# Optimization experiments

Measured on AMD Instinct MI355X. Metric: run time of the kernel, lower is better.

Reference implementation:

```python
import jax, jax.numpy as jnp
import numpy as np

EMBED = 1024
HEADS = 16
HDIM = EMBED // HEADS
WIN = 14
RANK = 16
ALPHA = 32
MLP = 4 * EMBED


def setup_inputs() -> dict:
    key = jax.random.key(0)
    ks = jax.random.split(key, 10)
    s = 0.02
    return {
        "x": jax.random.normal(ks[0], (2, 64, 64, EMBED), jnp.float32),
        "norm1_g": jnp.ones((EMBED,), jnp.float32),
        "norm1_b": jnp.zeros((EMBED,), jnp.float32),
        "qkv_w": jax.random.normal(ks[1], (EMBED, 3 * EMBED), jnp.float32) * s,
        "qkv_b": jnp.zeros((3 * EMBED,), jnp.float32),
        "lora_a": jax.random.normal(ks[2], (EMBED, RANK), jnp.float32) * s,
        "lora_b": jax.random.normal(ks[3], (RANK, 3 * EMBED), jnp.float32) * s,
        "rel_pos_h": jax.random.normal(ks[4], (2 * WIN - 1, HDIM), jnp.float32) * s,
        "rel_pos_w": jax.random.normal(ks[5], (2 * WIN - 1, HDIM), jnp.float32) * s,
        "proj_w": jax.random.normal(ks[6], (EMBED, EMBED), jnp.float32) * s,
        "proj_b": jnp.zeros((EMBED,), jnp.float32),
        "norm2_g": jnp.ones((EMBED,), jnp.float32),
        "norm2_b": jnp.zeros((EMBED,), jnp.float32),
        "mlp_w1": jax.random.normal(ks[7], (EMBED, MLP), jnp.float32) * s,
        "mlp_b1": jnp.zeros((MLP,), jnp.float32),
        "mlp_w2": jax.random.normal(ks[8], (MLP, EMBED), jnp.float32) * s,
        "mlp_b2": jnp.zeros((EMBED,), jnp.float32),
    }


def layer_norm(x, g, b, eps=1e-6):
    mu = jnp.mean(x, axis=-1, keepdims=True)
    var = jnp.var(x, axis=-1, keepdims=True)
    return (x - mu) * jax.lax.rsqrt(var + eps) * g + b


def window_partition(x, w):
    B, H, W, C = x.shape
    ph, pw = (w - H % w) % w, (w - W % w) % w
    x = jnp.pad(x, ((0, 0), (0, ph), (0, pw), (0, 0)))
    Hp, Wp = H + ph, W + pw
    x = x.reshape(B, Hp // w, w, Wp // w, w, C)
    x = x.transpose(0, 1, 3, 2, 4, 5).reshape(-1, w, w, C)
    return x, (Hp, Wp)


def window_unpartition(x, w, pad_hw, hw):
    Hp, Wp = pad_hw
    H, W = hw
    B = x.shape[0] // (Hp // w * (Wp // w))
    x = x.reshape(B, Hp // w, Wp // w, w, w, -1)
    x = x.transpose(0, 1, 3, 2, 4, 5).reshape(B, Hp, Wp, -1)
    return x[:, :H, :W, :]


def _rel_table(rel_pos, size):
    # square windows, no interpolation: table is (2*size-1, dim)
    idx = jnp.arange(size)[:, None] - jnp.arange(size)[None, :] + (size - 1)
    return rel_pos[idx]  # (size, size, dim)


def reference(x, norm1_g, norm1_b, qkv_w, qkv_b, lora_a, lora_b,
              rel_pos_h, rel_pos_w, proj_w, proj_b, norm2_g, norm2_b,
              mlp_w1, mlp_b1, mlp_w2, mlp_b2):
    shortcut = x
    xn = layer_norm(x, norm1_g, norm1_b)
    h, w = xn.shape[1], xn.shape[2]
    xw, pad_hw = window_partition(xn, WIN)
    Bw, H, W, C = xw.shape
    N = H * W
    xf = xw.reshape(Bw, N, C)
    # QKV with LoRA injection: qkv(x) + (x @ A @ B) * alpha/rank
    qkv = xf @ qkv_w + qkv_b + (xf @ lora_a @ lora_b) * (ALPHA / RANK)
    qkv = qkv.reshape(Bw, N, 3, HEADS, HDIM).transpose(2, 0, 3, 1, 4)  # 3,Bw,h,N,d
    q, k, v = qkv[0], qkv[1], qkv[2]
    scale = HDIM ** -0.5
    attn = jnp.einsum('bhnd,bhmd->bhnm', q * scale, k)  # (Bw,heads,N,N)
    # decomposed relative position bias
    Rh = _rel_table(rel_pos_h, H)  # (H,H,d)
    Rw = _rel_table(rel_pos_w, W)  # (W,W,d)
    rq = q.reshape(Bw, HEADS, H, W, HDIM)
    rel_h = jnp.einsum('bhxyd,xkd->bhxyk', rq, Rh)  # (Bw,heads,H,W,H)
    rel_w = jnp.einsum('bhxyd,ykd->bhxyk', rq, Rw)  # (Bw,heads,H,W,W)
    attn = (attn.reshape(Bw, HEADS, H, W, H, W)
            + rel_h[..., :, None] + rel_w[..., None, :]).reshape(Bw, HEADS, N, N)
    attn = jax.nn.softmax(attn, axis=-1)
    out = jnp.einsum('bhnm,bhmd->bhnd', attn, v)
    out = out.reshape(Bw, HEADS, H, W, HDIM).transpose(0, 2, 3, 1, 4).reshape(Bw, H, W, C)
    out = out @ proj_w + proj_b
    out = window_unpartition(out, WIN, pad_hw, (h, w))
    x = shortcut + out
    # MLP with exact GELU (torch default)
    xn2 = layer_norm(x, norm2_g, norm2_b)
    hmid = jax.nn.gelu(xn2 @ mlp_w1 + mlp_b1, approximate=False)
    x = x + (hmid @ mlp_w2 + mlp_b2)
    return x
```

## Files before the change

### kernel.cpp

```cpp
#include <hip/hip_runtime.h>
#include <cstdint>
#include <cstddef>


typedef __bf16 bf16x8 __attribute__((ext_vector_type(8)));
typedef float f32x4 __attribute__((ext_vector_type(4)));

__device__ __forceinline__ unsigned short f2bf(float f) {
    unsigned u = __float_as_uint(f);
    u = (u + 0x7fffu + ((u >> 16) & 1u)) >> 16;
    return (unsigned short)u;
}
__device__ __forceinline__ float bf2f(unsigned short h) {
    return __uint_as_float(((unsigned)h) << 16);
}

#define GLDS16(gp, lp) __builtin_amdgcn_global_load_lds( \
    (__attribute__((address_space(1))) unsigned int*)(gp), \
    (__attribute__((address_space(3))) unsigned int*)(lp), 16, 0, 0)

__global__ __launch_bounds__(256) void weff_kernel(
    const float* __restrict__ W, const float* __restrict__ la,
    const float* __restrict__ lb, unsigned short* __restrict__ Wt)
{
    __shared__ float tile[32][33];
    __shared__ float lat[32][16];
    __shared__ float lbt[16][32];
    const int kb = blockIdx.x * 32, nb = blockIdx.y * 32;
    const int tn = threadIdx.x & 31, tk = threadIdx.x >> 5;
    for (int i = threadIdx.x; i < 32 * 16; i += 256)
        lat[i >> 4][i & 15] = la[(size_t)(kb + (i >> 4)) * 16 + (i & 15)];
    for (int i = threadIdx.x; i < 16 * 32; i += 256)
        lbt[i >> 5][i & 31] = lb[(size_t)(i >> 5) * 3072 + nb + (i & 31)];
#pragma unroll
    for (int i = 0; i < 4; ++i) {
        int k = tk + i * 8;
        tile[k][tn] = W[(size_t)(kb + k) * 3072 + nb + tn];
    }
    __syncthreads();
#pragma unroll
    for (int i = 0; i < 4; ++i) {
        int n = tk + i * 8;
        float acc = tile[tn][n];
#pragma unroll
        for (int r = 0; r < 16; ++r) acc += 2.0f * lat[tn][r] * lbt[r][n];
        Wt[(size_t)(nb + n) * 1024 + kb + tn] = f2bf(acc);
    }
}

__global__ __launch_bounds__(256) void transpose_bf16_kernel(
    const float* __restrict__ W, unsigned short* __restrict__ Wt,
    int Kdim, int Ndim)
{
    __shared__ float tile[32][33];
    const int kb = blockIdx.x * 32, nb = blockIdx.y * 32;
    const int tn = threadIdx.x & 31, tk = threadIdx.x >> 5;
#pragma unroll
    for (int i = 0; i < 4; ++i) {
        int k = tk + i * 8;
        tile[k][tn] = W[(size_t)(kb + k) * Ndim + nb + tn];
    }
    __syncthreads();
#pragma unroll
    for (int i = 0; i < 4; ++i) {
        int n = tk + i * 8;
        Wt[(size_t)(nb + n) * Kdim + kb + tn] = f2bf(tile[tn][n]);
    }
}

__global__ __launch_bounds__(256) void ln1_kernel(
    const float* __restrict__ x, const float* __restrict__ g,
    const float* __restrict__ b, unsigned short* __restrict__ out)
{
    const int blk = blockIdx.x;
    const int tid = threadIdx.x;
    const int bw = blk / 196, tok = blk - bw * 196;
    const int bat = bw / 25, rw = bw - bat * 25;
    const int wy = rw / 5, wx = rw - wy * 5;
    const int ty = tok / 14, tx = tok - ty * 14;
    const int y = wy * 14 + ty, xx = wx * 14 + tx;
    unsigned short* orow = out + (size_t)blk * 1024;
    if (y >= 64 || xx >= 64) {
        *(uint2*)(orow + tid * 4) = make_uint2(0u, 0u);
        return;
    }
    const float* irow = x + ((size_t)((bat * 64 + y) * 64 + xx)) * 1024;
    const float4 v = *(const float4*)(irow + tid * 4);
    float s = v.x + v.y + v.z + v.w;
    float ss = v.x * v.x + v.y * v.y + v.z * v.z + v.w * v.w;
    for (int o = 32; o > 0; o >>= 1) { s += __shfl_xor(s, o); ss += __shfl_xor(ss, o); }
    __shared__ float red[8];
    const int wave = tid >> 6, lane = tid & 63;
    if (lane == 0) { red[wave] = s; red[4 + wave] = ss; }
    __syncthreads();
    s = red[0] + red[1] + red[2] + red[3];
    ss = red[4] + red[5] + red[6] + red[7];
    const float mu = s * (1.0f / 1024.0f);
    const float var = ss * (1.0f / 1024.0f) - mu * mu;
    const float rstd = rsqrtf(var + 1e-6f);
    const float4 gv = *(const float4*)(g + tid * 4);
    const float4 bv = *(const float4*)(b + tid * 4);
    const float a0 = (v.x - mu) * rstd * gv.x + bv.x;
    const float a1 = (v.y - mu) * rstd * gv.y + bv.y;
    const float a2 = (v.z - mu) * rstd * gv.z + bv.z;
    const float a3 = (v.w - mu) * rstd * gv.w + bv.w;
    const unsigned r0 = (unsigned)f2bf(a0) | ((unsigned)f2bf(a1) << 16);
    const unsigned r1 = (unsigned)f2bf(a2) | ((unsigned)f2bf(a3) << 16);
    *(uint2*)(orow + tid * 4) = make_uint2(r0, r1);
}

__global__ __launch_bounds__(256) void ln2_kernel(
    const float* __restrict__ x, const float* __restrict__ g,
    const float* __restrict__ b, unsigned short* __restrict__ out)
{
    const int blk = blockIdx.x;
    const int tid = threadIdx.x;
    const float* irow = x + (size_t)blk * 1024;
    unsigned short* orow = out + (size_t)blk * 1024;
    const float4 v = *(const float4*)(irow + tid * 4);
    float s = v.x + v.y + v.z + v.w;
    float ss = v.x * v.x + v.y * v.y + v.z * v.z + v.w * v.w;
    for (int o = 32; o > 0; o >>= 1) { s += __shfl_xor(s, o); ss += __shfl_xor(ss, o); }
    __shared__ float red[8];
    const int wave = tid >> 6, lane = tid & 63;
    if (lane == 0) { red[wave] = s; red[4 + wave] = ss; }
    __syncthreads();
    s = red[0] + red[1] + red[2] + red[3];
    ss = red[4] + red[5] + red[6] + red[7];
    const float mu = s * (1.0f / 1024.0f);
    const float var = ss * (1.0f / 1024.0f) - mu * mu;
    const float rstd = rsqrtf(var + 1e-6f);
    const float4 gv = *(const float4*)(g + tid * 4);
    const float4 bv = *(const float4*)(b + tid * 4);
    const float a0 = (v.x - mu) * rstd * gv.x + bv.x;
    const float a1 = (v.y - mu) * rstd * gv.y + bv.y;
    const float a2 = (v.z - mu) * rstd * gv.z + bv.z;
    const float a3 = (v.w - mu) * rstd * gv.w + bv.w;
    const unsigned r0 = (unsigned)f2bf(a0) | ((unsigned)f2bf(a1) << 16);
    const unsigned r1 = (unsigned)f2bf(a2) | ((unsigned)f2bf(a3) << 16);
    *(uint2*)(orow + tid * 4) = make_uint2(r0, r1);
}

template <int EPI, int KS>
__global__ __launch_bounds__(512, 2) void gemm8p_v3(
    const unsigned short* __restrict__ A,
    const unsigned short* __restrict__ Bt,
    const float* __restrict__ bias,
    void* __restrict__ outp,
    int M, int K, int nbm, int nbn)
{
    __shared__ unsigned short As_s[2 * 16384];
    __shared__ unsigned short Bs_s[2 * 16384];

    const int tid = threadIdx.x;
    const int wave = tid >> 6, lane = tid & 63;
    const int lr = lane & 15, lq = lane >> 4;

    const int ss = (nbm + 7) >> 3;
    const int xcd = blockIdx.x & 7;
    const int sidx = blockIdx.x >> 3;
    const int ntl2 = sidx / ss;
    const int m_loc = sidx - ntl2 * ss;
    const int mt = xcd * ss + m_loc;
    if (mt >= nbm) return;
    int ks = 0, ntl = ntl2;
    if constexpr (KS > 1) { ks = ntl2 / nbn; ntl = ntl2 - ks * nbn; }
    const int m_base = mt * 256, n_base = ntl * 256;
    const int Kp = K / KS, kb = ks * Kp;
    const int NT = Kp >> 6;

    const int wm = (wave >> 2) * 128;
    const int wn = (wave & 3) * 64;

    const int srow = tid >> 3, sslot = tid & 7;
    const int gch = sslot ^ (srow & 7);
    const unsigned short* a_gp[4];
    const unsigned short* b_gp[4];
#pragma unroll
    for (int u = 0; u < 4; ++u) {
        int ar = m_base + u * 64 + srow; ar = ar < M ? ar : M - 1;
        a_gp[u] = A + (size_t)ar * K + kb + gch * 8;
        b_gp[u] = Bt + (size_t)(n_base + u * 64 + srow) * K + kb + gch * 8;
    }
#define STG_A(t, u) GLDS16(a_gp[u] + (size_t)(t) * 64, As_s + (((t) & 1) << 14) + (u) * 4096 + tid * 8)
#define STG_B(t, u) GLDS16(b_gp[u] + (size_t)(t) * 64, Bs_s + (((t) & 1) << 14) + (u) * 4096 + tid * 8)

    const int sl0 = lq ^ (lr & 7);
    const int a_off = (wm + lr) * 64 + sl0 * 8;
    const int b_off = (wn + lr) * 64 + sl0 * 8;

    f32x4 acc[8][4] = {};

    STG_A(0, 0); STG_A(0, 2);
    STG_B(0, 0); STG_B(0, 1); STG_B(0, 2); STG_B(0, 3);
    STG_A(0, 1); STG_A(0, 3);
    asm volatile("s_waitcnt vmcnt(2)" ::: "memory");
    __builtin_amdgcn_s_barrier();

    for (int t = 0; t < NT; ++t) {
        const unsigned short* Ab = As_s + ((t & 1) << 14);
        const unsigned short* Bb = Bs_s + ((t & 1) << 14);
        bf16x8 af[4], bfv[4];
#pragma unroll
        for (int mf = 0; mf < 4; ++mf) af[mf] = *(const bf16x8*)(Ab + a_off + mf * 1024);
#pragma unroll
        for (int nf = 0; nf < 4; ++nf) bfv[nf] = *(const bf16x8*)(Bb + b_off + nf * 1024);
        if (t + 1 < NT) { STG_A(t + 1, 0); STG_A(t + 1, 2); }
        __builtin_amdgcn_s_barrier();
        asm volatile("s_waitcnt lgkmcnt(0)" ::: "memory");
        __builtin_amdgcn_sched_barrier(0);
        __builtin_amdgcn_s_setprio(1);
#pragma unroll
        for (int mf = 0; mf < 4; ++mf)
#pragma unroll
            for (int nf = 0; nf < 4; ++nf)
                acc[mf][nf] = __builtin_amdgcn_mfma_f32_16x16x32_bf16(af[mf], bfv[nf], acc[mf][nf], 0, 0, 0);
        __builtin_amdgcn_s_setprio(0);
        __builtin_amdgcn_s_barrier();
#pragma unroll
        for (int mf = 0; mf < 4; ++mf) af[mf] = *(const bf16x8*)(Ab + (a_off ^ 32) + mf * 1024);
#pragma unroll
        for (int nf = 0; nf < 4; ++nf) bfv[nf] = *(const bf16x8*)(Bb + (b_off ^ 32) + nf * 1024);
        if (t + 1 < NT) { STG_B(t + 1, 0); STG_B(t + 1, 1); }
        __builtin_amdgcn_s_barrier();
        asm volatile("s_waitcnt lgkmcnt(0)" ::: "memory");
        __builtin_amdgcn_sched_barrier(0);
        __builtin_amdgcn_s_setprio(1);
#pragma unroll
        for (int mf = 0; mf < 4; ++mf)
#pragma unroll
            for (int nf = 0; nf < 4; ++nf)
                acc[mf][nf] = __builtin_amdgcn_mfma_f32_16x16x32_bf16(af[mf], bfv[nf], acc[mf][nf], 0, 0, 0);
        __builtin_amdgcn_s_setprio(0);
        if (t == NT - 1) { asm volatile("s_waitcnt vmcnt(0)" ::: "memory"); }
        else             { asm volatile("s_waitcnt vmcnt(4)" ::: "memory"); }
        __builtin_amdgcn_s_barrier();
#pragma unroll
        for (int mf = 0; mf < 4; ++mf) af[mf] = *(const bf16x8*)(Ab + a_off + (4 + mf) * 1024);
#pragma unroll
        for (int nf = 0; nf < 4; ++nf) bfv[nf] = *(const bf16x8*)(Bb + b_off + nf * 1024);
        if (t + 1 < NT) { STG_B(t + 1, 2); STG_B(t + 1, 3); }
        __builtin_amdgcn_s_barrier();
        asm volatile("s_waitcnt lgkmcnt(0)" ::: "memory");
        __builtin_amdgcn_sched_barrier(0);
        __builtin_amdgcn_s_setprio(1);
#pragma unroll
        for (int mf = 0; mf < 4; ++mf)
#pragma unroll
            for (int nf = 0; nf < 4; ++nf)
                acc[4 + mf][nf] = __builtin_amdgcn_mfma_f32_16x16x32_bf16(af[mf], bfv[nf], acc[4 + mf][nf], 0, 0, 0);
        __builtin_amdgcn_s_setprio(0);
        __builtin_amdgcn_s_barrier();
#pragma unroll
        for (int mf = 0; mf < 4; ++mf) af[mf] = *(const bf16x8*)(Ab + (a_off ^ 32) + (4 + mf) * 1024);
#pragma unroll
        for (int nf = 0; nf < 4; ++nf) bfv[nf] = *(const bf16x8*)(Bb + (b_off ^ 32) + nf * 1024);
        if (t + 1 < NT) { STG_A(t + 1, 1); STG_A(t + 1, 3); }
        __builtin_amdgcn_s_barrier();
        asm volatile("s_waitcnt lgkmcnt(0)" ::: "memory");
        __builtin_amdgcn_sched_barrier(0);
        __builtin_amdgcn_s_setprio(1);
#pragma unroll
        for (int mf = 0; mf < 4; ++mf)
#pragma unroll
            for (int nf = 0; nf < 4; ++nf)
                acc[4 + mf][nf] = __builtin_amdgcn_mfma_f32_16x16x32_bf16(af[mf], bfv[nf], acc[4 + mf][nf], 0, 0, 0);
        __builtin_amdgcn_s_setprio(0);
        asm volatile("s_waitcnt vmcnt(2)" ::: "memory");
        __builtin_amdgcn_s_barrier();
    }
#undef STG_A
#undef STG_B

    float biasv[4];
#pragma unroll
    for (int j = 0; j < 4; ++j)
        biasv[j] = (KS == 1 || ks == 0) ? bias[n_base + wn + j * 16 + lr] : 0.0f;

    if constexpr (EPI == 0) {
#pragma unroll
        for (int i = 0; i < 8; ++i) {
            const int m0i = m_base + wm + i * 16 + lq * 4;
            if (m0i >= M) continue;
            const int bw = m0i / 196, tok0 = m0i - bw * 196;
#pragma unroll
            for (int j = 0; j < 4; ++j) {
                const int n = n_base + wn + j * 16 + lr;
                const int which = n >> 10, hh = (n >> 6) & 15, d = n & 63;
                unsigned short* slotp = (unsigned short*)outp + (size_t)((bw * 3 + which) * 16 + hh) * 13312;
                if (which == 2) {
                    unsigned long long pv = 0;
#pragma unroll
                    for (int r = 0; r < 4; ++r)
                        pv |= (unsigned long long)f2bf(acc[i][j][r] + biasv[j]) << (16 * r);
                    *(unsigned long long*)(slotp + (size_t)d * 208 + tok0) = pv;
                } else {
#pragma unroll
                    for (int r = 0; r < 4; ++r)
                        slotp[(size_t)(tok0 + r) * 64 + d] = f2bf(acc[i][j][r] + biasv[j]);
                }
            }
        }
    } else {
#pragma unroll
        for (int i = 0; i < 8; ++i) {
#pragma unroll
            for (int r = 0; r < 4; ++r) {
                const int m = m_base + wm + i * 16 + lq * 4 + r;
                if (m >= M) continue;
#pragma unroll
                for (int j = 0; j < 4; ++j) {
                    const int n = n_base + wn + j * 16 + lr;
                    const float v = acc[i][j][r] + biasv[j];
                    if constexpr (EPI == 2) {
                        const float t2 = 1.5957691216f * (v + 0.044715f * v * v * v);
                        const float e = __expf(-t2);
                        const float gl = v * __builtin_amdgcn_rcpf(1.0f + e);
                        ((unsigned short*)outp)[(size_t)m * 4096 + n] = f2bf(gl);
                    } else {
                        atomicAdd(&((float*)outp)[(size_t)m * 1024 + n], v);
                    }
                }
            }
        }
    }
}

template <int EPI>
__global__ __launch_bounds__(256) void gemm_kernel(
    const unsigned short* __restrict__ A,
    const unsigned short* __restrict__ Bt,
    const float* __restrict__ bias,
    void* __restrict__ outp,
    const float* __restrict__ aux,
    int M, int K, int nbm, int nbn)
{
    __shared__ unsigned short As[2][128 * 32];
    __shared__ unsigned short Bs[2][128 * 32];
    const int tid = threadIdx.x;
    const int wave = tid >> 6, lane = tid & 63;
    const int lr = lane & 15, lq = lane >> 4;
    const int ss = (nbm + 7) >> 3;
    const int xcd = blockIdx.x & 7;
    const int s = blockIdx.x >> 3;
    const int nt = s / ss;
    const int m_loc = s - nt * ss;
    const int mt = xcd * ss + m_loc;
    if (mt >= nbm) return;
    const int m_base = mt * 128, n_base = nt * 128;
    const int wm = (wave >> 1) * 64, wn = (wave & 1) * 64;
    const int N = nbn * 128;

    const int c0 = tid, c1 = tid + 256;
    const int row0 = c0 >> 2, row1 = c1 >> 2;
    const int kc = (tid & 3) ^ ((tid >> 3) & 3);
    int ar0 = m_base + row0; ar0 = ar0 < M ? ar0 : M - 1;
    int ar1 = m_base + row1; ar1 = ar1 < M ? ar1 : M - 1;
    int br0 = n_base + row0; br0 = br0 < N ? br0 : N - 1;
    int br1 = n_base + row1; br1 = br1 < N ? br1 : N - 1;
    const unsigned short* agp0 = A + (size_t)ar0 * K + kc * 8;
    const unsigned short* agp1 = A + (size_t)ar1 * K + kc * 8;
    const unsigned short* bgp0 = Bt + (size_t)br0 * K + kc * 8;
    const unsigned short* bgp1 = Bt + (size_t)br1 * K + kc * 8;
    unsigned short* alp0 = As[0] + c0 * 8;
    unsigned short* alp1 = As[0] + c1 * 8;
    unsigned short* blp0 = Bs[0] + c0 * 8;
    unsigned short* blp1 = Bs[0] + c1 * 8;
    unsigned short* alp0b = As[1] + c0 * 8;
    unsigned short* alp1b = As[1] + c1 * 8;
    unsigned short* blp0b = Bs[1] + c0 * 8;
    unsigned short* blp1b = Bs[1] + c1 * 8;

    const int swz = (lq ^ ((lr >> 1) & 3)) * 8;

    f32x4 acc[4][4] = {};

    for (int k0 = 0; k0 < K; k0 += 64) {
        GLDS16(agp0 + k0, alp0);
        GLDS16(agp1 + k0, alp1);
        GLDS16(bgp0 + k0, blp0);
        GLDS16(bgp1 + k0, blp1);
        GLDS16(agp0 + k0 + 32, alp0b);
        GLDS16(agp1 + k0 + 32, alp1b);
        GLDS16(bgp0 + k0 + 32, blp0b);
        GLDS16(bgp1 + k0 + 32, blp1b);
        __syncthreads();
#pragma unroll
        for (int half = 0; half < 2; ++half) {
            bf16x8 af[4], bfr[4];
#pragma unroll
            for (int i = 0; i < 4; ++i) {
                af[i]  = *(const bf16x8*)(As[half] + (wm + i * 16 + lr) * 32 + swz);
                bfr[i] = *(const bf16x8*)(Bs[half] + (wn + i * 16 + lr) * 32 + swz);
            }
#pragma unroll
            for (int i = 0; i < 4; ++i)
#pragma unroll
                for (int j = 0; j < 4; ++j)
                    acc[i][j] = __builtin_amdgcn_mfma_f32_16x16x32_bf16(af[i], bfr[j], acc[i][j], 0, 0, 0);
        }
        __syncthreads();
    }

    float biasv[4];
#pragma unroll
    for (int j = 0; j < 4; ++j) biasv[j] = bias[n_base + wn + j * 16 + lr];

#pragma unroll
    for (int i = 0; i < 4; ++i) {
#pragma unroll
        for (int r = 0; r < 4; ++r) {
            const int m = m_base + wm + i * 16 + lq * 4 + r;
            if (m >= M) continue;
            int y = 0, xx = 0, b = 0;
            if constexpr (EPI == 1) {
                const int bw = m / 196, tok = m - bw * 196;
                b = bw / 25;
                const int rw = bw - b * 25;
                const int wy = rw / 5, wx = rw - wy * 5;
                const int ty = tok / 14, tx = tok - ty * 14;
                y = wy * 14 + ty; xx = wx * 14 + tx;
            }
#pragma unroll
            for (int j = 0; j < 4; ++j) {
                const int n = n_base + wn + j * 16 + lr;
                const float v = acc[i][j][r] + biasv[j];
                if constexpr (EPI == 1) {
                    if (y < 64 && xx < 64) {
                        const size_t idx = ((size_t)((b * 64 + y) * 64 + xx)) * 1024 + n;
                        ((float*)outp)[idx] = aux[idx] + v;
                    }
                } else {
                    const size_t idx = (size_t)m * 1024 + n;
                    ((float*)outp)[idx] += v;
                }
            }
        }
    }
}

__global__ __launch_bounds__(256, 2) void attn_kernel(
    const unsigned short* __restrict__ qkv,
    const float* __restrict__ relh, const float* __restrict__ relw,
    unsigned short* __restrict__ attn_out)
{
    __shared__ unsigned short Vt[64][232];
    __shared__ unsigned short Pst[4][16][232];
    __shared__ unsigned short Db[196][28];

    const int tid = threadIdx.x;
    const int wave = tid >> 6, lane = tid & 63;
    const int lr = lane & 15, lq = lane >> 4;
    const int bw = blockIdx.x >> 4, h = blockIdx.x & 15;
    const unsigned short* qp = qkv + (size_t)((bw * 3 + 0) * 16 + h) * 13312;
    const unsigned short* kp = qkv + (size_t)((bw * 3 + 1) * 16 + h) * 13312;
    const unsigned short* vp = qkv + (size_t)((bw * 3 + 2) * 16 + h) * 13312;

    *(uint2*)&Pst[wave][lane >> 2][208 + (lane & 3) * 4] = make_uint2(0u, 0u);

    {
        unsigned short* vtf = &Vt[0][0];
        for (int idx = tid; idx < 64 * 29; idx += 256) {
            const int d = idx / 29, c = idx - d * 29;
            GLDS16(vp + d * 208 + c * 8, vtf + idx * 8);
        }
    }

    for (int t = wave; t < 28; t += 4) {
        const int isw = t >= 14;
        const int c = isw ? t - 14 : t;
        const int arow = isw ? (lr * 14 + c) : (c * 14 + lr);
        const unsigned short* ap = qp + arow * 64 + lq * 8;
        const bf16x8 a0 = *(const bf16x8*)ap;
        const bf16x8 a1 = *(const bf16x8*)(ap + 32);
        int ridx = c - lr + 13;
        ridx = ridx < 0 ? 0 : (ridx > 26 ? 26 : ridx);
        const float* tb = (isw ? relw : relh) + ridx * 64 + lq * 8;
        union BV { unsigned short u[8]; bf16x8 v; } b0, b1;
        {
            const float4 x0 = *(const float4*)tb;
            const float4 x1 = *(const float4*)(tb + 4);
            b0.u[0] = f2bf(x0.x); b0.u[1] = f2bf(x0.y); b0.u[2] = f2bf(x0.z); b0.u[3] = f2bf(x0.w);
            b0.u[4] = f2bf(x1.x); b0.u[5] = f2bf(x1.y); b0.u[6] = f2bf(x1.z); b0.u[7] = f2bf(x1.w);
            const float4 x2 = *(const float4*)(tb + 32);
            const float4 x3 = *(const float4*)(tb + 36);
            b1.u[0] = f2bf(x2.x); b1.u[1] = f2bf(x2.y); b1.u[2] = f2bf(x2.z); b1.u[3] = f2bf(x2.w);
            b1.u[4] = f2bf(x3.x); b1.u[5] = f2bf(x3.y); b1.u[6] = f2bf(x3.z); b1.u[7] = f2bf(x3.w);
        }
        f32x4 dacc = {};
        dacc = __builtin_amdgcn_mfma_f32_16x16x32_bf16(a0, b0.v, dacc, 0, 0, 0);
        dacc = __builtin_amdgcn_mfma_f32_16x16x32_bf16(a1, b1.v, dacc, 0, 0, 0);
#pragma unroll
        for (int r = 0; r < 4; ++r) {
            const int y = lq * 4 + r;
            if (y < 14 && lr < 14) {
                const int g = isw ? y * 14 + c : c * 14 + y;
                Db[g][isw ? 14 + lr : lr] = f2bf(dacc[r]);
            }
        }
    }
    __syncthreads();

    for (int mt = wave; mt < 13; mt += 4) {
        const int m0 = mt * 16;
        const unsigned short* qb = qp + (size_t)(m0 + lr) * 64 + lq * 8;
        const bf16x8 qa0 = *(const bf16x8*)qb;
        const bf16x8 qa1 = *(const bf16x8*)(qb + 32);
        f32x4 sc[13];
#pragma unroll
        for (int nt = 0; nt < 13; ++nt) {
            const unsigned short* kb = kp + (size_t)(nt * 16 + lr) * 64 + lq * 8;
            const bf16x8 k0 = *(const bf16x8*)kb;
            const bf16x8 k1 = *(const bf16x8*)(kb + 32);
            f32x4 a = {};
            a = __builtin_amdgcn_mfma_f32_16x16x32_bf16(qa0, k0, a, 0, 0, 0);
            a = __builtin_amdgcn_mfma_f32_16x16x32_bf16(qa1, k1, a, 0, 0, 0);
            sc[nt] = a;
        }
        int grow[4];
#pragma unroll
        for (int r = 0; r < 4; ++r) {
            int g = m0 + lq * 4 + r;
            grow[r] = g > 195 ? 195 : g;
        }
#pragma unroll
        for (int nt = 0; nt < 13; ++nt) {
            const int n = nt * 16 + lr;
            if (n < 196) {
                const int nx = n / 14, ny = n - nx * 14;
#pragma unroll
                for (int r = 0; r < 4; ++r)
                    sc[nt][r] = sc[nt][r] * 0.125f + bf2f(Db[grow[r]][nx]) + bf2f(Db[grow[r]][14 + ny]);
            } else {
#pragma unroll
                for (int r = 0; r < 4; ++r) sc[nt][r] = -1e30f;
            }
        }
        float rs[4];
#pragma unroll
        for (int r = 0; r < 4; ++r) {
            float mx = sc[0][r];
#pragma unroll
            for (int nt = 1; nt < 13; ++nt) mx = fmaxf(mx, sc[nt][r]);
            mx = fmaxf(mx, __shfl_xor(mx, 1));
            mx = fmaxf(mx, __shfl_xor(mx, 2));
            mx = fmaxf(mx, __shfl_xor(mx, 4));
            mx = fmaxf(mx, __shfl_xor(mx, 8));
            float s = 0.f;
#pragma unroll
            for (int nt = 0; nt < 13; ++nt) {
                const float e = __expf(sc[nt][r] - mx);
                sc[nt][r] = e;
                s += e;
            }
            s += __shfl_xor(s, 1);
            s += __shfl_xor(s, 2);
            s += __shfl_xor(s, 4);
            s += __shfl_xor(s, 8);
            rs[r] = 1.0f / s;
        }
#pragma unroll
        for (int nt = 0; nt < 13; ++nt)
#pragma unroll
            for (int r = 0; r < 4; ++r)
                Pst[wave][lq * 4 + r][nt * 16 + lr] = f2bf(sc[nt][r]);
#pragma unroll
        for (int dt = 0; dt < 4; ++dt) {
            f32x4 a = {};
#pragma unroll
            for (int ks = 0; ks < 7; ++ks) {
                const bf16x8 pa = *(const bf16x8*)&Pst[wave][lr][ks * 32 + lq * 8];
                const bf16x8 vb = *(const bf16x8*)&Vt[dt * 16 + lr][ks * 32 + lq * 8];
                a = __builtin_amdgcn_mfma_f32_16x16x32_bf16(pa, vb, a, 0, 0, 0);
            }
#pragma unroll
            for (int r = 0; r < 4; ++r) {
                const int m = m0 + lq * 4 + r;
                if (m < 196)
                    attn_out[(size_t)(bw * 196 + m) * 1024 + h * 64 + dt * 16 + lr] = f2bf(a[r] * rs[r]);
            }
        }
    }
}

extern "C" void kernel_launch(void* const* d_in, const int* in_sizes, int n_in,
                              void* d_out, int out_size, void* d_ws, size_t ws_size,
                              hipStream_t stream)
{
    (void)in_sizes; (void)n_in; (void)out_size; (void)ws_size;
    const float* x      = (const float*)d_in[0];
    const float* n1g    = (const float*)d_in[1];
    const float* n1b    = (const float*)d_in[2];
    const float* qkv_w  = (const float*)d_in[3];
    const float* qkv_b  = (const float*)d_in[4];
    const float* lora_a = (const float*)d_in[5];
    const float* lora_b = (const float*)d_in[6];
    const float* relh   = (const float*)d_in[7];
    const float* relw   = (const float*)d_in[8];
    const float* proj_w = (const float*)d_in[9];
    const float* proj_b = (const float*)d_in[10];
    const float* n2g    = (const float*)d_in[11];
    const float* n2b    = (const float*)d_in[12];
    const float* w1     = (const float*)d_in[13];
    const float* b1     = (const float*)d_in[14];
    const float* w2     = (const float*)d_in[15];
    const float* b2     = (const float*)d_in[16];
    float* out = (float*)d_out;

    char* ws = (char*)d_ws;
    size_t off = 0;
    auto alloc = [&](size_t bytes) {
        char* p = ws + off;
        off += (bytes + 255) & ~(size_t)255;
        return p;
    };
    unsigned short* weffT = (unsigned short*)alloc((size_t)3072 * 1024 * 2);
    unsigned short* projT = (unsigned short*)alloc((size_t)1024 * 1024 * 2);
    unsigned short* w1T   = (unsigned short*)alloc((size_t)4096 * 1024 * 2);
    unsigned short* w2T   = (unsigned short*)alloc((size_t)1024 * 4096 * 2);
    unsigned short* xnw   = (unsigned short*)alloc((size_t)9800 * 1024 * 2);
    unsigned short* qkvb  = (unsigned short*)alloc((size_t)8192 * 4096 * 2);
    unsigned short* attno = (unsigned short*)alloc((size_t)9800 * 1024 * 2);

    weff_kernel<<<dim3(32, 96), 256, 0, stream>>>(qkv_w, lora_a, lora_b, weffT);
    transpose_bf16_kernel<<<dim3(32, 32), 256, 0, stream>>>(proj_w, projT, 1024, 1024);
    transpose_bf16_kernel<<<dim3(32, 128), 256, 0, stream>>>(w1, w1T, 1024, 4096);
    transpose_bf16_kernel<<<dim3(128, 32), 256, 0, stream>>>(w2, w2T, 4096, 1024);
    ln1_kernel<<<9800, 256, 0, stream>>>(x, n1g, n1b, xnw);
    gemm8p_v3<0, 1><<<dim3(8 * 5 * 12), 512, 0, stream>>>(xnw, weffT, qkv_b, qkvb, 9800, 1024, 39, 12);
    attn_kernel<<<800, 256, 0, stream>>>(qkvb, relh, relw, attno);
    gemm_kernel<1><<<dim3(8 * 10 * 8), 256, 0, stream>>>(attno, projT, proj_b, out, x, 9800, 1024, 77, 8);
    unsigned short* xn2 = xnw;
    ln2_kernel<<<8192, 256, 0, stream>>>(out, n2g, n2b, xn2);
    unsigned short* hmid = qkvb;
    gemm8p_v3<2, 1><<<dim3(8 * 4 * 16), 512, 0, stream>>>(xn2, w1T, b1, hmid, 8192, 1024, 32, 16);
    gemm8p_v3<3, 2><<<dim3(8 * 4 * 8), 512, 0, stream>>>(hmid, w2T, b2, out, 8192, 4096, 32, 4);
}
```

Before: 574.3 us.

## Reorder 8-wave GEMM phases to reuse B fragments; move MLP2 to split-K 128x128 GEMM

The 256x256 8-wave GEMM's inner loop is reordered so that each B fragment loaded from LDS serves both M halves before the next K-half is read. This halves B-side LDS reads per tile, and the global-to-LDS stage issues and vmcnt waits are rearranged to match. Split-K support moves from that kernel to the 128x128 gemm_kernel, which now runs the MLP down-projection with split-K 2 and atomicAdd accumulation over 1024 blocks. The smaller tile improves occupancy and grid fill for that GEMM, but lowers data reuse per block and keeps the atomic traffic.

```diff
diff --git a/kernel.cpp b/kernel.cpp
--- a/kernel.cpp
+++ b/kernel.cpp
@@ -141,8 +141,8 @@
     *(uint2*)(orow + tid * 4) = make_uint2(r0, r1);
 }
 
-template <int EPI, int KS>
-__global__ __launch_bounds__(512, 2) void gemm8p_v3(
+template <int EPI>
+__global__ __launch_bounds__(512, 2) void gemm8p_v4(
     const unsigned short* __restrict__ A,
     const unsigned short* __restrict__ Bt,
     const float* __restrict__ bias,
@@ -159,15 +159,12 @@
     const int ss = (nbm + 7) >> 3;
     const int xcd = blockIdx.x & 7;
     const int sidx = blockIdx.x >> 3;
-    const int ntl2 = sidx / ss;
-    const int m_loc = sidx - ntl2 * ss;
+    const int ntl = sidx / ss;
+    const int m_loc = sidx - ntl * ss;
     const int mt = xcd * ss + m_loc;
     if (mt >= nbm) return;
-    int ks = 0, ntl = ntl2;
-    if constexpr (KS > 1) { ks = ntl2 / nbn; ntl = ntl2 - ks * nbn; }
     const int m_base = mt * 256, n_base = ntl * 256;
-    const int Kp = K / KS, kb = ks * Kp;
-    const int NT = Kp >> 6;
+    const int NT = K >> 6;
 
     const int wm = (wave >> 2) * 128;
     const int wn = (wave & 3) * 64;
@@ -179,8 +176,8 @@
 #pragma unroll
     for (int u = 0; u < 4; ++u) {
         int ar = m_base + u * 64 + srow; ar = ar < M ? ar : M - 1;
-        a_gp[u] = A + (size_t)ar * K + kb + gch * 8;
-        b_gp[u] = Bt + (size_t)(n_base + u * 64 + srow) * K + kb + gch * 8;
+        a_gp[u] = A + (size_t)ar * K + gch * 8;
+        b_gp[u] = Bt + (size_t)(n_base + u * 64 + srow) * K + gch * 8;
     }
 #define STG_A(t, u) GLDS16(a_gp[u] + (size_t)(t) * 64, As_s + (((t) & 1) << 14) + (u) * 4096 + tid * 8)
 #define STG_B(t, u) GLDS16(b_gp[u] + (size_t)(t) * 64, Bs_s + (((t) & 1) << 14) + (u) * 4096 + tid * 8)
@@ -191,8 +188,8 @@
 
     f32x4 acc[8][4] = {};
 
+    STG_B(0, 0); STG_B(0, 1); STG_B(0, 2); STG_B(0, 3);
     STG_A(0, 0); STG_A(0, 2);
-    STG_B(0, 0); STG_B(0, 1); STG_B(0, 2); STG_B(0, 3);
     STG_A(0, 1); STG_A(0, 3);
     asm volatile("s_waitcnt vmcnt(2)" ::: "memory");
     __builtin_amdgcn_s_barrier();
@@ -205,22 +202,6 @@
         for (int mf = 0; mf < 4; ++mf) af[mf] = *(const bf16x8*)(Ab + a_off + mf * 1024);
 #pragma unroll
         for (int nf = 0; nf < 4; ++nf) bfv[nf] = *(const bf16x8*)(Bb + b_off + nf * 1024);
-        if (t + 1 < NT) { STG_A(t + 1, 0); STG_A(t + 1, 2); }
-        __builtin_amdgcn_s_barrier();
-        asm volatile("s_waitcnt lgkmcnt(0)" ::: "memory");
-        __builtin_amdgcn_sched_barrier(0);
-        __builtin_amdgcn_s_setprio(1);
-#pragma unroll
-        for (int mf = 0; mf < 4; ++mf)
-#pragma unroll
-            for (int nf = 0; nf < 4; ++nf)
-                acc[mf][nf] = __builtin_amdgcn_mfma_f32_16x16x32_bf16(af[mf], bfv[nf], acc[mf][nf], 0, 0, 0);
-        __builtin_amdgcn_s_setprio(0);
-        __builtin_amdgcn_s_barrier();
-#pragma unroll
-        for (int mf = 0; mf < 4; ++mf) af[mf] = *(const bf16x8*)(Ab + (a_off ^ 32) + mf * 1024);
-#pragma unroll
-        for (int nf = 0; nf < 4; ++nf) bfv[nf] = *(const bf16x8*)(Bb + (b_off ^ 32) + nf * 1024);
         if (t + 1 < NT) { STG_B(t + 1, 0); STG_B(t + 1, 1); }
         __builtin_amdgcn_s_barrier();
         asm volatile("s_waitcnt lgkmcnt(0)" ::: "memory");
@@ -233,12 +214,10 @@
                 acc[mf][nf] = __builtin_amdgcn_mfma_f32_16x16x32_bf16(af[mf], bfv[nf], acc[mf][nf], 0, 0, 0);
         __builtin_amdgcn_s_setprio(0);
         if (t == NT - 1) { asm volatile("s_waitcnt vmcnt(0)" ::: "memory"); }
-        else             { asm volatile("s_waitcnt vmcnt(4)" ::: "memory"); }
+        else             { asm volatile("s_waitcnt vmcnt(2)" ::: "memory"); }
         __builtin_amdgcn_s_barrier();
 #pragma unroll
         for (int mf = 0; mf < 4; ++mf) af[mf] = *(const bf16x8*)(Ab + a_off + (4 + mf) * 1024);
-#pragma unroll
-        for (int nf = 0; nf < 4; ++nf) bfv[nf] = *(const bf16x8*)(Bb + b_off + nf * 1024);
         if (t + 1 < NT) { STG_B(t + 1, 2); STG_B(t + 1, 3); }
         __builtin_amdgcn_s_barrier();
         asm volatile("s_waitcnt lgkmcnt(0)" ::: "memory");
@@ -252,10 +231,10 @@
         __builtin_amdgcn_s_setprio(0);
         __builtin_amdgcn_s_barrier();
 #pragma unroll
-        for (int mf = 0; mf < 4; ++mf) af[mf] = *(const bf16x8*)(Ab + (a_off ^ 32) + (4 + mf) * 1024);
+        for (int mf = 0; mf < 4; ++mf) af[mf] = *(const bf16x8*)(Ab + (a_off ^ 32) + mf * 1024);
 #pragma unroll
         for (int nf = 0; nf < 4; ++nf) bfv[nf] = *(const bf16x8*)(Bb + (b_off ^ 32) + nf * 1024);
-        if (t + 1 < NT) { STG_A(t + 1, 1); STG_A(t + 1, 3); }
+        if (t + 1 < NT) { STG_A(t + 1, 0); STG_A(t + 1, 2); }
         __builtin_amdgcn_s_barrier();
         asm volatile("s_waitcnt lgkmcnt(0)" ::: "memory");
         __builtin_amdgcn_sched_barrier(0);
@@ -264,9 +243,23 @@
         for (int mf = 0; mf < 4; ++mf)
 #pragma unroll
             for (int nf = 0; nf < 4; ++nf)
+                acc[mf][nf] = __builtin_amdgcn_mfma_f32_16x16x32_bf16(af[mf], bfv[nf], acc[mf][nf], 0, 0, 0);
+        __builtin_amdgcn_s_setprio(0);
+        __builtin_amdgcn_s_barrier();
+#pragma unroll
+        for (int mf = 0; mf < 4; ++mf) af[mf] = *(const bf16x8*)(Ab + (a_off ^ 32) + (4 + mf) * 1024);
+        if (t + 1 < NT) { STG_A(t + 1, 1); STG_A(t + 1, 3); }
+        __builtin_amdgcn_s_barrier();
+        asm volatile("s_waitcnt lgkmcnt(0)" ::: "memory");
+        __builtin_amdgcn_sched_barrier(0);
+        __builtin_amdgcn_s_setprio(1);
+#pragma unroll
+        for (int mf = 0; mf < 4; ++mf)
+#pragma unroll
+            for (int nf = 0; nf < 4; ++nf)
                 acc[4 + mf][nf] = __builtin_amdgcn_mfma_f32_16x16x32_bf16(af[mf], bfv[nf], acc[4 + mf][nf], 0, 0, 0);
         __builtin_amdgcn_s_setprio(0);
-        asm volatile("s_waitcnt vmcnt(2)" ::: "memory");
+        if (t < NT - 1) { asm volatile("s_waitcnt vmcnt(2)" ::: "memory"); }
         __builtin_amdgcn_s_barrier();
     }
 #undef STG_A
@@ -274,8 +267,7 @@
 
     float biasv[4];
 #pragma unroll
-    for (int j = 0; j < 4; ++j)
-        biasv[j] = (KS == 1 || ks == 0) ? bias[n_base + wn + j * 16 + lr] : 0.0f;
+    for (int j = 0; j < 4; ++j) biasv[j] = bias[n_base + wn + j * 16 + lr];
 
     if constexpr (EPI == 0) {
 #pragma unroll
@@ -312,21 +304,17 @@
                 for (int j = 0; j < 4; ++j) {
                     const int n = n_base + wn + j * 16 + lr;
                     const float v = acc[i][j][r] + biasv[j];
-                    if constexpr (EPI == 2) {
-                        const float t2 = 1.5957691216f * (v + 0.044715f * v * v * v);
-                        const float e = __expf(-t2);
-                        const float gl = v * __builtin_amdgcn_rcpf(1.0f + e);
-                        ((unsigned short*)outp)[(size_t)m * 4096 + n] = f2bf(gl);
-                    } else {
-                        atomicAdd(&((float*)outp)[(size_t)m * 1024 + n], v);
-                    }
+                    const float t2 = 1.5957691216f * (v + 0.044715f * v * v * v);
+                    const float e = __expf(-t2);
+                    const float gl = v * __builtin_amdgcn_rcpf(1.0f + e);
+                    ((unsigned short*)outp)[(size_t)m * 4096 + n] = f2bf(gl);
                 }
             }
         }
     }
 }
 
-template <int EPI>
+template <int EPI, int KS>
 __global__ __launch_bounds__(256) void gemm_kernel(
     const unsigned short* __restrict__ A,
     const unsigned short* __restrict__ Bt,
@@ -343,11 +331,14 @@
     const int ss = (nbm + 7) >> 3;
     const int xcd = blockIdx.x & 7;
     const int s = blockIdx.x >> 3;
-    const int nt = s / ss;
-    const int m_loc = s - nt * ss;
+    const int nt2 = s / ss;
+    const int m_loc = s - nt2 * ss;
     const int mt = xcd * ss + m_loc;
     if (mt >= nbm) return;
+    int ks = 0, nt = nt2;
+    if constexpr (KS > 1) { ks = nt2 / nbn; nt = nt2 - ks * nbn; }
     const int m_base = mt * 128, n_base = nt * 128;
+    const int Kp = K / KS, kbase = ks * Kp;
     const int wm = (wave >> 1) * 64, wn = (wave & 1) * 64;
     const int N = nbn * 128;
 
@@ -358,10 +349,10 @@
     int ar1 = m_base + row1; ar1 = ar1 < M ? ar1 : M - 1;
     int br0 = n_base + row0; br0 = br0 < N ? br0 : N - 1;
     int br1 = n_base + row1; br1 = br1 < N ? br1 : N - 1;
-    const unsigned short* agp0 = A + (size_t)ar0 * K + kc * 8;
-    const unsigned short* agp1 = A + (size_t)ar1 * K + kc * 8;
-    const unsigned short* bgp0 = Bt + (size_t)br0 * K + kc * 8;
-    const unsigned short* bgp1 = Bt + (size_t)br1 * K + kc * 8;
+    const unsigned short* agp0 = A + (size_t)ar0 * K + kbase + kc * 8;
+    const unsigned short* agp1 = A + (size_t)ar1 * K + kbase + kc * 8;
+    const unsigned short* bgp0 = Bt + (size_t)br0 * K + kbase + kc * 8;
+    const unsigned short* bgp1 = Bt + (size_t)br1 * K + kbase + kc * 8;
     unsigned short* alp0 = As[0] + c0 * 8;
     unsigned short* alp1 = As[0] + c1 * 8;
     unsigned short* blp0 = Bs[0] + c0 * 8;
@@ -375,7 +366,7 @@
 
     f32x4 acc[4][4] = {};
 
-    for (int k0 = 0; k0 < K; k0 += 64) {
+    for (int k0 = 0; k0 < Kp; k0 += 64) {
         GLDS16(agp0 + k0, alp0);
         GLDS16(agp1 + k0, alp1);
         GLDS16(bgp0 + k0, blp0);
@@ -404,7 +395,8 @@
 
     float biasv[4];
 #pragma unroll
-    for (int j = 0; j < 4; ++j) biasv[j] = bias[n_base + wn + j * 16 + lr];
+    for (int j = 0; j < 4; ++j)
+        biasv[j] = (KS == 1 || ks == 0) ? bias[n_base + wn + j * 16 + lr] : 0.0f;
 
 #pragma unroll
     for (int i = 0; i < 4; ++i) {
@@ -432,7 +424,8 @@
                     }
                 } else {
                     const size_t idx = (size_t)m * 1024 + n;
-                    ((float*)outp)[idx] += v;
+                    if constexpr (KS > 1) atomicAdd(&((float*)outp)[idx], v);
+                    else                  ((float*)outp)[idx] += v;
                 }
             }
         }
@@ -627,12 +620,12 @@
     transpose_bf16_kernel<<<dim3(32, 128), 256, 0, stream>>>(w1, w1T, 1024, 4096);
     transpose_bf16_kernel<<<dim3(128, 32), 256, 0, stream>>>(w2, w2T, 4096, 1024);
     ln1_kernel<<<9800, 256, 0, stream>>>(x, n1g, n1b, xnw);
-    gemm8p_v3<0, 1><<<dim3(8 * 5 * 12), 512, 0, stream>>>(xnw, weffT, qkv_b, qkvb, 9800, 1024, 39, 12);
+    gemm8p_v4<0><<<dim3(8 * 5 * 12), 512, 0, stream>>>(xnw, weffT, qkv_b, qkvb, 9800, 1024, 39, 12);
     attn_kernel<<<800, 256, 0, stream>>>(qkvb, relh, relw, attno);
-    gemm_kernel<1><<<dim3(8 * 10 * 8), 256, 0, stream>>>(attno, projT, proj_b, out, x, 9800, 1024, 77, 8);
+    gemm_kernel<1, 1><<<dim3(8 * 10 * 8), 256, 0, stream>>>(attno, projT, proj_b, out, x, 9800, 1024, 77, 8);
     unsigned short* xn2 = xnw;
     ln2_kernel<<<8192, 256, 0, stream>>>(out, n2g, n2b, xn2);
     unsigned short* hmid = qkvb;
-    gemm8p_v3<2, 1><<<dim3(8 * 4 * 16), 512, 0, stream>>>(xn2, w1T, b1, hmid, 8192, 1024, 32, 16);
-    gemm8p_v3<3, 2><<<dim3(8 * 4 * 8), 512, 0, stream>>>(hmid, w2T, b2, out, 8192, 4096, 32, 4);
-}
+    gemm8p_v4<2><<<dim3(8 * 4 * 16), 512, 0, stream>>>(xn2, w1T, b1, hmid, 8192, 1024, 32, 16);
+    gemm_kernel<3, 2><<<dim3(8 * 8 * 16), 256, 0, stream>>>(hmid, w2T, b2, out, nullptr, 8192, 4096, 64, 8);
+}
```

New measurement: 588.8 us. 1.03x slower.
